# Kernel tuning notes

Measured on AMD Instinct MI355X. Metric: run time of the kernel, lower is better.

Reference implementation:

```python
import jax, jax.numpy as jnp
import numpy as np

B, N, C_IN = 16, 4096, 64
NPOINT = 1024
RADII = (0.2, 0.4)
NSAMPLES = (32, 64)
MLPS = ((64, 64, 128), (64, 64, 128))
C_TOTAL = sum(m[-1] for m in MLPS)


def setup_inputs() -> dict:
    key = jax.random.key(0)
    ks = jax.random.split(key, 24)
    inp = {
        "xyz": jax.random.uniform(ks[0], (B, N, 3), jnp.float32),
        "features": jax.random.normal(ks[1], (B, N, C_IN), jnp.float32),
        "w_att": jax.random.normal(ks[2], (3 * NPOINT, C_TOTAL), jnp.float32) * 0.02,
        "b_att": jnp.zeros((C_TOTAL,), jnp.float32),
    }
    k = 3
    for g, mlp in enumerate(MLPS):
        cin = 3 + C_IN
        for l, cout in enumerate(mlp):
            inp[f"w{g}_{l}"] = jax.random.normal(ks[k], (cout, cin), jnp.float32) * (1.0 / np.sqrt(cin))
            inp[f"b{g}_{l}"] = jnp.zeros((cout,), jnp.float32)
            k += 1
            cin = cout
    return inp


def _fps(xyz, npoint):
    # furthest point sampling; xyz (B,N,3) -> idx (B,npoint) int32. First idx is 0 (matches CUDA op).
    b, n, _ = xyz.shape
    init_idx = jnp.zeros((b,), jnp.int32)
    init_dist = jnp.full((b, n), 1e10, xyz.dtype)

    def body(carry, _):
        dists, last = carry
        last_pt = jnp.take_along_axis(xyz, last[:, None, None].astype(jnp.int32), axis=1)  # (B,1,3)
        d = jnp.sum((xyz - last_pt) ** 2, axis=-1)  # (B,N)
        dists = jnp.minimum(dists, d)
        nxt = jnp.argmax(dists, axis=-1).astype(jnp.int32)
        return (dists, nxt), nxt

    (_, _), rest = jax.lax.scan(body, (init_dist, init_idx), None, length=npoint - 1)
    return jnp.concatenate([init_idx[None, :], rest], axis=0).T  # (B, npoint)


def _ball_query(radius, nsample, xyz, new_xyz):
    # first-nsample points of xyz within radius of each new_xyz center (slots padded with first hit)
    n = xyz.shape[1]
    d2 = jnp.sum((new_xyz[:, :, None, :] - xyz[:, None, :, :]) ** 2, axis=-1)  # (B,S,N)
    mask = d2 < radius * radius
    order_key = jnp.where(mask, jnp.arange(n, dtype=jnp.int32)[None, None, :], n)
    idx = jnp.argsort(order_key, axis=-1)[..., :nsample].astype(jnp.int32)  # (B,S,nsample)
    valid = jnp.take_along_axis(mask, idx, axis=-1)
    return jnp.where(valid, idx, idx[..., :1])


def _group(xyz, new_xyz, features, idx):
    # -> (B, 3+C, S, nsample): relative xyz concat grouped features
    b, s, ns = idx.shape
    flat = idx.reshape(b, s * ns)
    gx = jnp.take_along_axis(xyz, flat[..., None], axis=1).reshape(b, s, ns, 3)
    gx = gx - new_xyz[:, :, None, :]
    gf = jnp.take_along_axis(features, flat[..., None], axis=1).reshape(b, s, ns, features.shape[-1])
    return jnp.transpose(jnp.concatenate([gx, gf], axis=-1), (0, 3, 1, 2))


def reference(xyz, features, w_att, b_att,
              w0_0, b0_0, w0_1, b0_1, w0_2, b0_2,
              w1_0, b1_0, w1_1, b1_1, w1_2, b1_2):
    xyz_sg = jax.lax.stop_gradient(xyz)  # index selection is non-differentiable (matches CUDA ops)
    fps_idx = _fps(xyz_sg, NPOINT)  # (B, npoint)
    new_xyz = jnp.take_along_axis(xyz, fps_idx[..., None], axis=1)  # (B, npoint, 3)

    # attention gate from sampled coordinates: (B, 3, npoint) flattened -> (B, C_TOTAL)
    att_in = jnp.transpose(new_xyz, (0, 2, 1)).reshape(xyz.shape[0], 3 * NPOINT)
    att = jax.nn.sigmoid(att_in @ w_att + b_att)  # (B, C_TOTAL)

    layer_sets = (((w0_0, b0_0), (w0_1, b0_1), (w0_2, b0_2)),
                  ((w1_0, b1_0), (w1_1, b1_1), (w1_2, b1_2)))
    pooled = []
    new_xyz_sg = jax.lax.stop_gradient(new_xyz)
    for radius, ns, layers in zip(RADII, NSAMPLES, layer_sets):
        idx = _ball_query(radius, ns, xyz_sg, new_xyz_sg)
        x = _group(xyz, new_xyz, features, idx)  # (B, 3+C, S, ns)
        for w, b in layers:  # shared 1x1 conv + ReLU per layer
            x = jax.nn.relu(jnp.einsum('oc,bcsn->bosn', w, x) + b[None, :, None, None])
        pooled.append(jnp.max(x, axis=-1))  # max over nsample -> (B, cout, S)

    features_cat = jnp.concatenate(pooled, axis=1)  # (B, C_TOTAL, S)
    features_end = features_cat * att[:, :, None]
    return new_xyz, features_end
```

## Files before the change

kernel.cpp:

```cpp
#include <hip/hip_runtime.h>
#include <cstdint>
#include <cstddef>


constexpr int B_ = 16, N_ = 4096, S_ = 1024;
constexpr int WT_G = 67*64 + 64*64 + 128*64 + 64 + 64 + 128;
constexpr int FPS_T = 512;
constexpr int WT_BLK = (2*WT_G + FPS_T - 1) / FPS_T;
constexpr int G1_BLK = 2 * B_ * (N_ / 128);

constexpr int WS_XYZF = 0;
constexpr int WS_NXYZ = B_*N_*4;
constexpr int WS_ATT  = WS_NXYZ + B_*S_*3;
constexpr int WS_WT   = WS_ATT + B_*256;
constexpr int WS_IDX0 = WS_WT + 2*WT_G;
constexpr int WS_IDX1 = WS_IDX0 + B_*S_*32;
constexpr int WS_F1   = WS_IDX1 + B_*S_*64;

__global__ __launch_bounds__(256) void g1_kernel(
    const float* __restrict__ xyz, const float* __restrict__ feats,
    const float* __restrict__ w00, const float* __restrict__ w10,
    float* __restrict__ f1) {
  __shared__ float wfs[67 * 64];
  const int fid = blockIdx.x;
  const int g = fid >> 9, b = (fid >> 5) & 15, chunk = fid & 31;
  const float* w = g ? w10 : w00;
  for (int k = threadIdx.x; k < 67*64; k += 256) {
    int c = k >> 6, o = k & 63;
    wfs[k] = w[o*67 + c];
  }
  __syncthreads();
  const int p = chunk * 128 + (threadIdx.x >> 1);
  const int half = (threadIdx.x & 1) * 32;
  const float* xr = xyz + ((size_t)b * N_ + p) * 3;
  const float* fr = feats + ((size_t)b * N_ + p) * 64;
  float acc[32];
  {
    float x0 = xr[0], x1 = xr[1], x2 = xr[2];
#pragma unroll
    for (int j = 0; j < 32; j += 4) {
      float4 wA = *(const float4*)&wfs[0*64 + half + j];
      acc[j+0] = wA.x * x0; acc[j+1] = wA.y * x0;
      acc[j+2] = wA.z * x0; acc[j+3] = wA.w * x0;
    }
#pragma unroll
    for (int j = 0; j < 32; j += 4) {
      float4 wA = *(const float4*)&wfs[1*64 + half + j];
      acc[j+0] = fmaf(wA.x, x1, acc[j+0]); acc[j+1] = fmaf(wA.y, x1, acc[j+1]);
      acc[j+2] = fmaf(wA.z, x1, acc[j+2]); acc[j+3] = fmaf(wA.w, x1, acc[j+3]);
    }
#pragma unroll
    for (int j = 0; j < 32; j += 4) {
      float4 wA = *(const float4*)&wfs[2*64 + half + j];
      acc[j+0] = fmaf(wA.x, x2, acc[j+0]); acc[j+1] = fmaf(wA.y, x2, acc[j+1]);
      acc[j+2] = fmaf(wA.z, x2, acc[j+2]); acc[j+3] = fmaf(wA.w, x2, acc[j+3]);
    }
  }
  for (int c = 0; c < 64; ++c) {
    float v = fr[c];
    const float* wr = &wfs[(3 + c) * 64 + half];
#pragma unroll
    for (int j = 0; j < 32; j += 4) {
      float4 w4 = *(const float4*)&wr[j];
      acc[j+0] = fmaf(w4.x, v, acc[j+0]); acc[j+1] = fmaf(w4.y, v, acc[j+1]);
      acc[j+2] = fmaf(w4.z, v, acc[j+2]); acc[j+3] = fmaf(w4.w, v, acc[j+3]);
    }
  }
  float* op = f1 + (((size_t)g * B_ + b) * N_ + p) * 64 + half;
#pragma unroll
  for (int j = 0; j < 32; j += 4) {
    float4 r = make_float4(acc[j], acc[j+1], acc[j+2], acc[j+3]);
    *(float4*)&op[j] = r;
  }
}

__global__ __launch_bounds__(512) void fps_wt_kernel(
    const float* __restrict__ xyz,
    const float* __restrict__ w00, const float* __restrict__ w01,
    const float* __restrict__ w02, const float* __restrict__ b00,
    const float* __restrict__ b01, const float* __restrict__ b02,
    const float* __restrict__ w10, const float* __restrict__ w11,
    const float* __restrict__ w12, const float* __restrict__ b10,
    const float* __restrict__ b11, const float* __restrict__ b12,
    float4* __restrict__ xyzf, float* __restrict__ wt,
    float* __restrict__ nxyz, float* __restrict__ out_nxyz) {
  constexpr int PPT = 8;
  __shared__ float sx[N_*3];
  __shared__ int   selidx[S_];
  __shared__ alignas(16) unsigned long long redP[2][8];

  if (blockIdx.x >= B_) {
    int wid = (blockIdx.x - B_) * FPS_T + threadIdx.x;
    if (wid >= 2*WT_G) return;
    int g = wid / WT_G, r = wid % WT_G;
    float val;
    if (r < 4288) {
      int c = r >> 6, o = r & 63;
      val = (g ? w10 : w00)[o*67 + c];
    } else if (r < 8384) {
      int rr = r - 4288; int c = rr >> 6, o = rr & 63;
      val = (g ? w11 : w01)[o*64 + c];
    } else if (r < 16576) {
      int rr = r - 8384; int c = rr >> 7, o = rr & 127;
      val = (g ? w12 : w02)[o*64 + c];
    } else {
      int rr = r - 16576;
      val = (rr < 64)  ? (g ? b10 : b00)[rr]
          : (rr < 128) ? (g ? b11 : b01)[rr - 64]
                       : (g ? b12 : b02)[rr - 128];
    }
    wt[g*WT_G + r] = val;
    return;
  }

  const int b = blockIdx.x, t = threadIdx.x;
  const int wv = t >> 6;
  const float* xr = xyz + (size_t)b * N_ * 3;
  for (int k = t; k < N_*3; k += FPS_T) sx[k] = xr[k];
  if (t == 0) selidx[0] = 0;
  __syncthreads();
  float px[PPT], py[PPT], pz[PPT], m[PPT];
#pragma unroll
  for (int p = 0; p < PPT; ++p) {
    int idx = t * PPT + p;
    px[p] = sx[idx*3+0]; py[p] = sx[idx*3+1]; pz[p] = sx[idx*3+2];
    m[p] = 1e10f;
  }
  float lx = sx[0], ly = sx[1], lz = sx[2];
  for (int i = 1; i < S_; ++i) {
#pragma unroll
    for (int p = 0; p < PPT; ++p) {
      float dx = __fsub_rn(px[p], lx), dy = __fsub_rn(py[p], ly), dz = __fsub_rn(pz[p], lz);
      float d = __fadd_rn(__fadd_rn(__fmul_rn(dx,dx), __fmul_rn(dy,dy)), __fmul_rn(dz,dz));
      m[p] = fminf(m[p], d);
    }
    float h0 = fmaxf(fmaxf(m[0], m[1]), fmaxf(m[2], m[3]));
    float h1 = fmaxf(fmaxf(m[4], m[5]), fmaxf(m[6], m[7]));
    float bv = fmaxf(h0, h1);
    int bp = PPT - 1;
#pragma unroll
    for (int p = PPT - 2; p >= 0; --p)
      if (m[p] == bv) bp = p;
    const int bi = t * PPT + bp;
    unsigned vm = __float_as_uint(bv);
#define DPP_MAX(ctrl) { unsigned o = (unsigned)__builtin_amdgcn_update_dpp((int)vm, (int)vm, (ctrl), 0xf, 0xf, false); vm = vm > o ? vm : o; }
    DPP_MAX(0x111)
    DPP_MAX(0x112)
    DPP_MAX(0x114)
    DPP_MAX(0x118)
    DPP_MAX(0x142)
    DPP_MAX(0x143)
#undef DPP_MAX
    const unsigned wmaxu = (unsigned)__builtin_amdgcn_readlane((int)vm, 63);
    const unsigned long long mk = __ballot(__float_as_uint(bv) == wmaxu);
    const int fl = (int)__builtin_ctzll(mk);
    const int widx = __builtin_amdgcn_readlane(bi, fl);
    const int par = i & 1;
    if (t == (widx >> 3))
      redP[par][wv] = ((unsigned long long)wmaxu << 32) | (unsigned)(~widx);
    __syncthreads();
    ulonglong2 pA = *(const ulonglong2*)&redP[par][0];
    ulonglong2 pB = *(const ulonglong2*)&redP[par][2];
    ulonglong2 pC = *(const ulonglong2*)&redP[par][4];
    ulonglong2 pD = *(const ulonglong2*)&redP[par][6];
    unsigned long long q0 = pA.x > pA.y ? pA.x : pA.y;
    unsigned long long q1 = pB.x > pB.y ? pB.x : pB.y;
    unsigned long long q2 = pC.x > pC.y ? pC.x : pC.y;
    unsigned long long q3 = pD.x > pD.y ? pD.x : pD.y;
    unsigned long long r0 = q0 > q1 ? q0 : q1;
    unsigned long long r1 = q2 > q3 ? q2 : q3;
    unsigned long long win = r0 > r1 ? r0 : r1;
    const int fi = (int)(~(unsigned)win);
    lx = sx[fi*3+0]; ly = sx[fi*3+1]; lz = sx[fi*3+2];
    if (t == 0) selidx[i] = fi;
  }
  __syncthreads();
  for (int k = t; k < S_; k += FPS_T) {
    int id = selidx[k];
    float x = sx[id*3], y = sx[id*3+1], z = sx[id*3+2];
    int o = (b * S_ + k) * 3;
    nxyz[o] = x; nxyz[o+1] = y; nxyz[o+2] = z;
    out_nxyz[o] = x; out_nxyz[o+1] = y; out_nxyz[o+2] = z;
  }
  for (int k = t; k < N_; k += FPS_T) {
    float4 v; v.x = sx[k*3]; v.y = sx[k*3+1]; v.z = sx[k*3+2]; v.w = 0.f;
    xyzf[b * N_ + k] = v;
  }
}

__global__ __launch_bounds__(256) void ballq_att_kernel(
    const float4* __restrict__ xyzf, const float* __restrict__ nxyz,
    int* __restrict__ idx0buf, int* __restrict__ idx1buf,
    const float* __restrict__ w_att, const float* __restrict__ b_att,
    float* __restrict__ att) {
  __shared__ float ai[3 * S_];
  if (blockIdx.x >= B_*S_/4) {
    int b = blockIdx.x - B_*S_/4, t = threadIdx.x;
    for (int k = t; k < 3 * S_; k += 256) {
      int d = k >> 10, s = k & 1023;
      ai[k] = nxyz[(b * S_ + s) * 3 + d];
    }
    __syncthreads();
    float acc = b_att[t];
#pragma unroll 8
    for (int k = 0; k < 3 * S_; ++k)
      acc = fmaf(ai[k], w_att[k * 256 + t], acc);
    att[b * 256 + t] = 1.f / (1.f + expf(-acc));
    return;
  }
  const float r2a = (float)(0.2 * 0.2), r2b = (float)(0.4 * 0.4);
  int lane = threadIdx.x & 63;
  int cid = blockIdx.x * 4 + (threadIdx.x >> 6);
  int b = cid >> 10;
  float cx = nxyz[cid*3], cy = nxyz[cid*3+1], cz = nxyz[cid*3+2];
  const float4* xb = xyzf + b * N_;
  int cnt0 = 0, cnt1 = 0, first0 = 0, first1 = 0;
  const unsigned long long below = (1ull << lane) - 1ull;
  for (int base = 0; base < N_; base += 64) {
    float4 P = xb[base + lane];
    float dx = __fsub_rn(cx, P.x), dy = __fsub_rn(cy, P.y), dz = __fsub_rn(cz, P.z);
    float d2 = __fadd_rn(__fadd_rn(__fmul_rn(dx,dx), __fmul_rn(dy,dy)), __fmul_rn(dz,dz));
    bool h0 = d2 < r2a, h1 = d2 < r2b;
    unsigned long long m0 = __ballot(h0), m1 = __ballot(h1);
    if (cnt0 == 0 && m0 != 0ull) first0 = base + (int)__builtin_ctzll(m0);
    if (cnt1 == 0 && m1 != 0ull) first1 = base + (int)__builtin_ctzll(m1);
    if (h0) {
      int pos = cnt0 + (int)__popcll(m0 & below);
      if (pos < 32) idx0buf[cid * 32 + pos] = base + lane;
    }
    if (h1) {
      int pos = cnt1 + (int)__popcll(m1 & below);
      if (pos < 64) idx1buf[cid * 64 + pos] = base + lane;
    }
    cnt0 += (int)__popcll(m0);
    cnt1 += (int)__popcll(m1);
    if (cnt0 >= 32 && cnt1 >= 64) break;
  }
  if (cnt0 < 32)
    for (int p = cnt0 + lane; p < 32; p += 64) idx0buf[cid * 32 + p] = first0;
  if (cnt1 < 64)
    for (int p = cnt1 + lane; p < 64; p += 64) idx1buf[cid * 64 + p] = first1;
}

template<int NS>
__device__ __forceinline__ void mlp_body(int bi, float* xs,
    const float* __restrict__ f1g,
    const float* __restrict__ nxyz, const float* __restrict__ att,
    const int* __restrict__ idxbuf, const float* __restrict__ wt,
    float* __restrict__ outf, int g) {
  constexpr int NCEN = 128 / NS;
  constexpr int XS = 132;
  float* red = xs;
  const int t = threadIdx.x;
  const int cid0 = bi * NCEN;
  const int b = cid0 >> 10;

  const float* w0  = wt;
  const float* w1  = wt + 67*64;
  const float* w2  = w1 + 64*64;
  const float* bb0 = w2 + 64*128;
  const float* bb1 = bb0 + 64;
  const float* bb2 = bb1 + 64;

  const int og = t & 15, cg = t >> 4;
  float acc[4][8];

  {
    const int col0 = cg * 8;
    const int cidg = cid0 + col0 / NS;
    const int jb = cidg * NS + (col0 % NS);
    const int4 pA = *(const int4*)&idxbuf[jb];
    const int4 pB = *(const int4*)&idxbuf[jb + 4];
    int pc[8] = {pA.x, pA.y, pA.z, pA.w, pB.x, pB.y, pB.z, pB.w};
    const float nx = nxyz[cidg*3], ny = nxyz[cidg*3+1], nz = nxyz[cidg*3+2];
    const float4 bv = *(const float4*)&bb0[og*4];
    float bc[4];
#pragma unroll
    for (int j = 0; j < 4; ++j) {
      const int o = og*4 + j;
      float c1 = fmaf(w0[128+o], nz, fmaf(w0[64+o], ny, w0[o]*nx));
      bc[j] = ((const float*)&bv)[j] - c1;
    }
#pragma unroll
    for (int cc = 0; cc < 8; ++cc) {
      float4 fv = *(const float4*)&f1g[((size_t)b * N_ + pc[cc]) * 64 + og*4];
      acc[0][cc] = bc[0] + fv.x;
      acc[1][cc] = bc[1] + fv.y;
      acc[2][cc] = bc[2] + fv.z;
      acc[3][cc] = bc[3] + fv.w;
    }
  }
#pragma unroll
  for (int oo = 0; oo < 4; ++oo) {
    float4 y0, y1;
    y0.x=fmaxf(acc[oo][0],0.f); y0.y=fmaxf(acc[oo][1],0.f);
    y0.z=fmaxf(acc[oo][2],0.f); y0.w=fmaxf(acc[oo][3],0.f);
    y1.x=fmaxf(acc[oo][4],0.f); y1.y=fmaxf(acc[oo][5],0.f);
    y1.z=fmaxf(acc[oo][6],0.f); y1.w=fmaxf(acc[oo][7],0.f);
    *(float4*)&xs[(og*4+oo)*XS + cg*8]     = y0;
    *(float4*)&xs[(og*4+oo)*XS + cg*8 + 4] = y1;
  }
  __syncthreads();

  {
    float4 bv = *(const float4*)&bb1[og*4];
    float b4[4] = {bv.x, bv.y, bv.z, bv.w};
#pragma unroll
    for (int oo = 0; oo < 4; ++oo)
#pragma unroll
      for (int cc = 0; cc < 8; ++cc) acc[oo][cc] = b4[oo];
#pragma unroll 2
    for (int k = 0; k < 64; ++k) {
      float4 x0 = *(const float4*)&xs[k*XS + cg*8];
      float4 x1 = *(const float4*)&xs[k*XS + cg*8 + 4];
      float4 wv = *(const float4*)&w1[k*64 + og*4];
      float x8[8] = {x0.x,x0.y,x0.z,x0.w,x1.x,x1.y,x1.z,x1.w};
      float w4[4] = {wv.x,wv.y,wv.z,wv.w};
#pragma unroll
      for (int oo = 0; oo < 4; ++oo)
#pragma unroll
        for (int cc = 0; cc < 8; ++cc) acc[oo][cc] = fmaf(w4[oo], x8[cc], acc[oo][cc]);
    }
  }
  __syncthreads();
#pragma unroll
  for (int oo = 0; oo < 4; ++oo) {
    float4 y0, y1;
    y0.x=fmaxf(acc[oo][0],0.f); y0.y=fmaxf(acc[oo][1],0.f);
    y0.z=fmaxf(acc[oo][2],0.f); y0.w=fmaxf(acc[oo][3],0.f);
    y1.x=fmaxf(acc[oo][4],0.f); y1.y=fmaxf(acc[oo][5],0.f);
    y1.z=fmaxf(acc[oo][6],0.f); y1.w=fmaxf(acc[oo][7],0.f);
    *(float4*)&xs[(og*4+oo)*XS + cg*8]     = y0;
    *(float4*)&xs[(og*4+oo)*XS + cg*8 + 4] = y1;
  }
  __syncthreads();

  float acc3[8][8];
  {
    float4 b0v = *(const float4*)&bb2[og*8];
    float4 b1v = *(const float4*)&bb2[og*8 + 4];
    float b8[8] = {b0v.x,b0v.y,b0v.z,b0v.w,b1v.x,b1v.y,b1v.z,b1v.w};
#pragma unroll
    for (int oo = 0; oo < 8; ++oo)
#pragma unroll
      for (int cc = 0; cc < 8; ++cc) acc3[oo][cc] = b8[oo];
#pragma unroll 2
    for (int k = 0; k < 64; ++k) {
      float4 x0 = *(const float4*)&xs[k*XS + cg*8];
      float4 x1 = *(const float4*)&xs[k*XS + cg*8 + 4];
      float4 wa = *(const float4*)&w2[k*128 + og*8];
      float4 wb = *(const float4*)&w2[k*128 + og*8 + 4];
      float x8[8] = {x0.x,x0.y,x0.z,x0.w,x1.x,x1.y,x1.z,x1.w};
      float w8[8] = {wa.x,wa.y,wa.z,wa.w,wb.x,wb.y,wb.z,wb.w};
#pragma unroll
      for (int oo = 0; oo < 8; ++oo)
#pragma unroll
        for (int cc = 0; cc < 8; ++cc) acc3[oo][cc] = fmaf(w8[oo], x8[cc], acc3[oo][cc]);
    }
  }
  float pm[8];
#pragma unroll
  for (int oo = 0; oo < 8; ++oo) {
    float v = fmaxf(acc3[oo][0], 0.f);
#pragma unroll
    for (int cc = 1; cc < 8; ++cc) v = fmaxf(v, fmaxf(acc3[oo][cc], 0.f));
    pm[oo] = v;
  }
#pragma unroll
  for (int oo = 0; oo < 8; ++oo) {
    pm[oo] = fmaxf(pm[oo], __shfl_xor(pm[oo], 16));
    pm[oo] = fmaxf(pm[oo], __shfl_xor(pm[oo], 32));
  }
  __syncthreads();
  if ((t & 63) < 16) {
    int w = t >> 6;
#pragma unroll
    for (int oo = 0; oo < 8; ++oo) red[w*128 + og*8 + oo] = pm[oo];
  }
  __syncthreads();

  const int ch = t & 127;
  const float a = att[b*256 + g*128 + ch];
  if (NS == 64) {
    int c = t >> 7;
    float v = fmaxf(red[(2*c)*128 + ch], red[(2*c+1)*128 + ch]);
    int s = (cid0 + c) & 1023;
    outf[((size_t)(b*256 + g*128 + ch)) * 1024 + s] = v * a;
  } else {
#pragma unroll
    for (int kk = 0; kk < 2; ++kk) {
      int c = (t >> 7) * 2 + kk;
      float v = red[c*128 + ch];
      int s = (cid0 + c) & 1023;
      outf[((size_t)(b*256 + g*128 + ch)) * 1024 + s] = v * a;
    }
  }
}

__global__ __launch_bounds__(256, 4) void mlp_kernel(
    const float* __restrict__ f1, const float* __restrict__ nxyz,
    const float* __restrict__ att, const int* __restrict__ idx0,
    const int* __restrict__ idx1, const float* __restrict__ wt,
    float* __restrict__ outf) {
  constexpr int XS = 132;
  __shared__ float xs[64 * XS];
  if (blockIdx.x < 4096)
    mlp_body<32>(blockIdx.x, xs, f1, nxyz, att, idx0, wt, outf, 0);
  else
    mlp_body<64>(blockIdx.x - 4096, xs, f1 + (size_t)B_*N_*64,
                 nxyz, att, idx1, wt + WT_G, outf, 1);
}

extern "C" void kernel_launch(void* const* d_in, const int* in_sizes, int n_in,
                              void* d_out, int out_size, void* d_ws, size_t ws_size,
                              hipStream_t stream) {
  const float* xyz   = (const float*)d_in[0];
  const float* feats = (const float*)d_in[1];
  const float* w_att = (const float*)d_in[2];
  const float* b_att = (const float*)d_in[3];
  const float* w00 = (const float*)d_in[4];
  const float* b00 = (const float*)d_in[5];
  const float* w01 = (const float*)d_in[6];
  const float* b01 = (const float*)d_in[7];
  const float* w02 = (const float*)d_in[8];
  const float* b02 = (const float*)d_in[9];
  const float* w10 = (const float*)d_in[10];
  const float* b10 = (const float*)d_in[11];
  const float* w11 = (const float*)d_in[12];
  const float* b11 = (const float*)d_in[13];
  const float* w12 = (const float*)d_in[14];
  const float* b12 = (const float*)d_in[15];

  float* wsf = (float*)d_ws;
  int*   wsi = (int*)d_ws;
  float4* xyzf = (float4*)(wsf + WS_XYZF);
  float* nxyz  = wsf + WS_NXYZ;
  float* att   = wsf + WS_ATT;
  float* wt    = wsf + WS_WT;
  int* idx0 = wsi + WS_IDX0;
  int* idx1 = wsi + WS_IDX1;
  float* f1 = wsf + WS_F1;

  float* out  = (float*)d_out;
  float* outf = out + B_ * S_ * 3;

  hipLaunchKernelGGL(g1_kernel, dim3(G1_BLK), dim3(256), 0, stream,
                     xyz, feats, w00, w10, f1);
  hipLaunchKernelGGL(fps_wt_kernel, dim3(B_ + WT_BLK), dim3(FPS_T), 0, stream,
                     xyz, w00, w01, w02, b00, b01, b02, w10, w11, w12,
                     b10, b11, b12, xyzf, wt, nxyz, out);
  hipLaunchKernelGGL(ballq_att_kernel, dim3(B_*S_/4 + B_), dim3(256), 0, stream,
                     xyzf, nxyz, idx0, idx1, w_att, b_att, att);
  hipLaunchKernelGGL(mlp_kernel, dim3(12288), dim3(256), 0, stream,
                     f1, nxyz, att, idx0, idx1, wt, outf);
}
```

Measured before the change: 1.276 ms.

## Double MLP block tile to 256 columns per block with 16 columns per thread

Each MLP block now processes 256 grouped samples instead of 128, so each thread computes a 4x16 / 8x16 register tile and the shared-memory row stride grows to 260. Weight loads from global and LDS are amortized over twice as many columns, and the grid is halved. The max-pool reduction is reworked because one wave now spans two centers for radius 0.2. The cost is higher register pressure (launch bounds lowered from 4 to 2 blocks per SM), larger LDS use and lower occupancy, which may hurt latency hiding on the gathered feature loads.

```diff
diff --git a/kernel.cpp b/kernel.cpp
--- a/kernel.cpp
+++ b/kernel.cpp
@@ -8,6 +8,8 @@
 constexpr int FPS_T = 512;
 constexpr int WT_BLK = (2*WT_G + FPS_T - 1) / FPS_T;
 constexpr int G1_BLK = 2 * B_ * (N_ / 128);
+constexpr int MLP_B0 = B_ * S_ / 8;
+constexpr int MLP_B1 = B_ * S_ / 4;
 
 constexpr int WS_XYZF = 0;
 constexpr int WS_NXYZ = B_*N_*4;
@@ -248,8 +250,8 @@
     const float* __restrict__ nxyz, const float* __restrict__ att,
     const int* __restrict__ idxbuf, const float* __restrict__ wt,
     float* __restrict__ outf, int g) {
-  constexpr int NCEN = 128 / NS;
-  constexpr int XS = 132;
+  constexpr int NCEN = 256 / NS;
+  constexpr int XS = 260;
   float* red = xs;
   const int t = threadIdx.x;
   const int cid0 = bi * NCEN;
@@ -263,15 +265,18 @@
   const float* bb2 = bb1 + 64;
 
   const int og = t & 15, cg = t >> 4;
-  float acc[4][8];
+  float acc[4][16];
 
   {
-    const int col0 = cg * 8;
+    const int col0 = cg * 16;
     const int cidg = cid0 + col0 / NS;
     const int jb = cidg * NS + (col0 % NS);
     const int4 pA = *(const int4*)&idxbuf[jb];
     const int4 pB = *(const int4*)&idxbuf[jb + 4];
-    int pc[8] = {pA.x, pA.y, pA.z, pA.w, pB.x, pB.y, pB.z, pB.w};
+    const int4 pC = *(const int4*)&idxbuf[jb + 8];
+    const int4 pD = *(const int4*)&idxbuf[jb + 12];
+    int pc[16] = {pA.x,pA.y,pA.z,pA.w, pB.x,pB.y,pB.z,pB.w,
+                  pC.x,pC.y,pC.z,pC.w, pD.x,pD.y,pD.z,pD.w};
     const float nx = nxyz[cidg*3], ny = nxyz[cidg*3+1], nz = nxyz[cidg*3+2];
     const float4 bv = *(const float4*)&bb0[og*4];
     float bc[4];
@@ -282,7 +287,7 @@
       bc[j] = ((const float*)&bv)[j] - c1;
     }
 #pragma unroll
-    for (int cc = 0; cc < 8; ++cc) {
+    for (int cc = 0; cc < 16; ++cc) {
       float4 fv = *(const float4*)&f1g[((size_t)b * N_ + pc[cc]) * 64 + og*4];
       acc[0][cc] = bc[0] + fv.x;
       acc[1][cc] = bc[1] + fv.y;
@@ -291,15 +296,14 @@
     }
   }
 #pragma unroll
-  for (int oo = 0; oo < 4; ++oo) {
-    float4 y0, y1;
-    y0.x=fmaxf(acc[oo][0],0.f); y0.y=fmaxf(acc[oo][1],0.f);
-    y0.z=fmaxf(acc[oo][2],0.f); y0.w=fmaxf(acc[oo][3],0.f);
-    y1.x=fmaxf(acc[oo][4],0.f); y1.y=fmaxf(acc[oo][5],0.f);
-    y1.z=fmaxf(acc[oo][6],0.f); y1.w=fmaxf(acc[oo][7],0.f);
-    *(float4*)&xs[(og*4+oo)*XS + cg*8]     = y0;
-    *(float4*)&xs[(og*4+oo)*XS + cg*8 + 4] = y1;
-  }
+  for (int oo = 0; oo < 4; ++oo)
+#pragma unroll
+    for (int q = 0; q < 4; ++q) {
+      float4 y;
+      y.x=fmaxf(acc[oo][q*4+0],0.f); y.y=fmaxf(acc[oo][q*4+1],0.f);
+      y.z=fmaxf(acc[oo][q*4+2],0.f); y.w=fmaxf(acc[oo][q*4+3],0.f);
+      *(float4*)&xs[(og*4+oo)*XS + cg*16 + q*4] = y;
+    }
   __syncthreads();
 
   {
@@ -308,34 +312,36 @@
 #pragma unroll
     for (int oo = 0; oo < 4; ++oo)
 #pragma unroll
-      for (int cc = 0; cc < 8; ++cc) acc[oo][cc] = b4[oo];
+      for (int cc = 0; cc < 16; ++cc) acc[oo][cc] = b4[oo];
 #pragma unroll 2
     for (int k = 0; k < 64; ++k) {
-      float4 x0 = *(const float4*)&xs[k*XS + cg*8];
-      float4 x1 = *(const float4*)&xs[k*XS + cg*8 + 4];
+      float4 x0 = *(const float4*)&xs[k*XS + cg*16];
+      float4 x1 = *(const float4*)&xs[k*XS + cg*16 + 4];
+      float4 x2 = *(const float4*)&xs[k*XS + cg*16 + 8];
+      float4 x3 = *(const float4*)&xs[k*XS + cg*16 + 12];
       float4 wv = *(const float4*)&w1[k*64 + og*4];
-      float x8[8] = {x0.x,x0.y,x0.z,x0.w,x1.x,x1.y,x1.z,x1.w};
+      float x16[16] = {x0.x,x0.y,x0.z,x0.w, x1.x,x1.y,x1.z,x1.w,
+                       x2.x,x2.y,x2.z,x2.w, x3.x,x3.y,x3.z,x3.w};
       float w4[4] = {wv.x,wv.y,wv.z,wv.w};
 #pragma unroll
       for (int oo = 0; oo < 4; ++oo)
 #pragma unroll
-        for (int cc = 0; cc < 8; ++cc) acc[oo][cc] = fmaf(w4[oo], x8[cc], acc[oo][cc]);
-    }
-  }
-  __syncthreads();
-#pragma unroll
-  for (int oo = 0; oo < 4; ++oo) {
-    float4 y0, y1;
-    y0.x=fmaxf(acc[oo][0],0.f); y0.y=fmaxf(acc[oo][1],0.f);
-    y0.z=fmaxf(acc[oo][2],0.f); y0.w=fmaxf(acc[oo][3],0.f);
-    y1.x=fmaxf(acc[oo][4],0.f); y1.y=fmaxf(acc[oo][5],0.f);
-    y1.z=fmaxf(acc[oo][6],0.f); y1.w=fmaxf(acc[oo][7],0.f);
-    *(float4*)&xs[(og*4+oo)*XS + cg*8]     = y0;
-    *(float4*)&xs[(og*4+oo)*XS + cg*8 + 4] = y1;
-  }
-  __syncthreads();
-
-  float acc3[8][8];
+        for (int cc = 0; cc < 16; ++cc) acc[oo][cc] = fmaf(w4[oo], x16[cc], acc[oo][cc]);
+    }
+  }
+  __syncthreads();
+#pragma unroll
+  for (int oo = 0; oo < 4; ++oo)
+#pragma unroll
+    for (int q = 0; q < 4; ++q) {
+      float4 y;
+      y.x=fmaxf(acc[oo][q*4+0],0.f); y.y=fmaxf(acc[oo][q*4+1],0.f);
+      y.z=fmaxf(acc[oo][q*4+2],0.f); y.w=fmaxf(acc[oo][q*4+3],0.f);
+      *(float4*)&xs[(og*4+oo)*XS + cg*16 + q*4] = y;
+    }
+  __syncthreads();
+
+  float acc3[8][16];
   {
     float4 b0v = *(const float4*)&bb2[og*8];
     float4 b1v = *(const float4*)&bb2[og*8 + 4];
@@ -343,19 +349,22 @@
 #pragma unroll
     for (int oo = 0; oo < 8; ++oo)
 #pragma unroll
-      for (int cc = 0; cc < 8; ++cc) acc3[oo][cc] = b8[oo];
+      for (int cc = 0; cc < 16; ++cc) acc3[oo][cc] = b8[oo];
 #pragma unroll 2
     for (int k = 0; k < 64; ++k) {
-      float4 x0 = *(const float4*)&xs[k*XS + cg*8];
-      float4 x1 = *(const float4*)&xs[k*XS + cg*8 + 4];
+      float4 x0 = *(const float4*)&xs[k*XS + cg*16];
+      float4 x1 = *(const float4*)&xs[k*XS + cg*16 + 4];
+      float4 x2 = *(const float4*)&xs[k*XS + cg*16 + 8];
+      float4 x3 = *(const float4*)&xs[k*XS + cg*16 + 12];
       float4 wa = *(const float4*)&w2[k*128 + og*8];
       float4 wb = *(const float4*)&w2[k*128 + og*8 + 4];
-      float x8[8] = {x0.x,x0.y,x0.z,x0.w,x1.x,x1.y,x1.z,x1.w};
+      float x16[16] = {x0.x,x0.y,x0.z,x0.w, x1.x,x1.y,x1.z,x1.w,
+                       x2.x,x2.y,x2.z,x2.w, x3.x,x3.y,x3.z,x3.w};
       float w8[8] = {wa.x,wa.y,wa.z,wa.w,wb.x,wb.y,wb.z,wb.w};
 #pragma unroll
       for (int oo = 0; oo < 8; ++oo)
 #pragma unroll
-        for (int cc = 0; cc < 8; ++cc) acc3[oo][cc] = fmaf(w8[oo], x8[cc], acc3[oo][cc]);
+        for (int cc = 0; cc < 16; ++cc) acc3[oo][cc] = fmaf(w8[oo], x16[cc], acc3[oo][cc]);
     }
   }
   float pm[8];
@@ -363,30 +372,46 @@
   for (int oo = 0; oo < 8; ++oo) {
     float v = fmaxf(acc3[oo][0], 0.f);
 #pragma unroll
-    for (int cc = 1; cc < 8; ++cc) v = fmaxf(v, fmaxf(acc3[oo][cc], 0.f));
+    for (int cc = 1; cc < 16; ++cc) v = fmaxf(v, fmaxf(acc3[oo][cc], 0.f));
     pm[oo] = v;
   }
-#pragma unroll
-  for (int oo = 0; oo < 8; ++oo) {
-    pm[oo] = fmaxf(pm[oo], __shfl_xor(pm[oo], 16));
-    pm[oo] = fmaxf(pm[oo], __shfl_xor(pm[oo], 32));
-  }
-  __syncthreads();
-  if ((t & 63) < 16) {
-    int w = t >> 6;
-#pragma unroll
-    for (int oo = 0; oo < 8; ++oo) red[w*128 + og*8 + oo] = pm[oo];
-  }
-  __syncthreads();
-
-  const int ch = t & 127;
-  const float a = att[b*256 + g*128 + ch];
-  if (NS == 64) {
-    int c = t >> 7;
-    float v = fmaxf(red[(2*c)*128 + ch], red[(2*c+1)*128 + ch]);
-    int s = (cid0 + c) & 1023;
-    outf[((size_t)(b*256 + g*128 + ch)) * 1024 + s] = v * a;
+  const int lane = t & 63;
+  if (NS == 32) {
+#pragma unroll
+    for (int oo = 0; oo < 8; ++oo)
+      pm[oo] = fmaxf(pm[oo], __shfl_xor(pm[oo], 16));
+    __syncthreads();
+    if ((lane & 31) < 16) {
+      int w = t >> 6;
+      int crow = 2*w + (lane >> 5);
+#pragma unroll
+      for (int oo = 0; oo < 8; ++oo) red[crow*128 + og*8 + oo] = pm[oo];
+    }
+    __syncthreads();
+    const int ch = t & 127;
+    const float a = att[b*256 + g*128 + ch];
+#pragma unroll
+    for (int kk = 0; kk < 4; ++kk) {
+      int c = (t >> 7) * 4 + kk;
+      float v = red[c*128 + ch];
+      int s = (cid0 + c) & 1023;
+      outf[((size_t)(b*256 + g*128 + ch)) * 1024 + s] = v * a;
+    }
   } else {
+#pragma unroll
+    for (int oo = 0; oo < 8; ++oo) {
+      pm[oo] = fmaxf(pm[oo], __shfl_xor(pm[oo], 16));
+      pm[oo] = fmaxf(pm[oo], __shfl_xor(pm[oo], 32));
+    }
+    __syncthreads();
+    if (lane < 16) {
+      int w = t >> 6;
+#pragma unroll
+      for (int oo = 0; oo < 8; ++oo) red[w*128 + og*8 + oo] = pm[oo];
+    }
+    __syncthreads();
+    const int ch = t & 127;
+    const float a = att[b*256 + g*128 + ch];
 #pragma unroll
     for (int kk = 0; kk < 2; ++kk) {
       int c = (t >> 7) * 2 + kk;
@@ -397,17 +422,17 @@
   }
 }
 
-__global__ __launch_bounds__(256, 4) void mlp_kernel(
+__global__ __launch_bounds__(256, 2) void mlp_kernel(
     const float* __restrict__ f1, const float* __restrict__ nxyz,
     const float* __restrict__ att, const int* __restrict__ idx0,
     const int* __restrict__ idx1, const float* __restrict__ wt,
     float* __restrict__ outf) {
-  constexpr int XS = 132;
+  constexpr int XS = 260;
   __shared__ float xs[64 * XS];
-  if (blockIdx.x < 4096)
+  if (blockIdx.x < MLP_B0)
     mlp_body<32>(blockIdx.x, xs, f1, nxyz, att, idx0, wt, outf, 0);
   else
-    mlp_body<64>(blockIdx.x - 4096, xs, f1 + (size_t)B_*N_*64,
+    mlp_body<64>(blockIdx.x - MLP_B0, xs, f1 + (size_t)B_*N_*64,
                  nxyz, att, idx1, wt + WT_G, outf, 1);
 }
 
@@ -451,6 +476,6 @@
                      b10, b11, b12, xyzf, wt, nxyz, out);
   hipLaunchKernelGGL(ballq_att_kernel, dim3(B_*S_/4 + B_), dim3(256), 0, stream,
                      xyzf, nxyz, idx0, idx1, w_att, b_att, att);
-  hipLaunchKernelGGL(mlp_kernel, dim3(12288), dim3(256), 0, stream,
+  hipLaunchKernelGGL(mlp_kernel, dim3(MLP_B0 + MLP_B1), dim3(256), 0, stream,
                      f1, nxyz, att, idx0, idx1, wt, outf);
 }
```

Result: no change. 1.281 ms (+0.4%).
